# Kernel optimization log

Hardware: AMD Instinct MI355X
Metric: run time of the kernel (lower is better)

Reference implementation:

```python
import jax, jax.numpy as jnp
import numpy as np

MODEL_DIM = 1024
NUM_HEADS = 16
HEAD_DIM = MODEL_DIM // NUM_HEADS
B, N = 4, 2048


def setup_inputs() -> dict:
    key = jax.random.key(0)
    ks = jax.random.split(key, 6)
    s = 1.0 / np.sqrt(MODEL_DIM)
    x = jax.random.normal(ks[0], (B, N, MODEL_DIM), dtype=jnp.float32)
    Wq = jax.random.uniform(ks[1], (MODEL_DIM, MODEL_DIM), jnp.float32, -s, s)
    Wk = jax.random.uniform(ks[2], (MODEL_DIM, MODEL_DIM), jnp.float32, -s, s)
    Wv = jax.random.uniform(ks[3], (MODEL_DIM, MODEL_DIM), jnp.float32, -s, s)
    Wo = jax.random.uniform(ks[4], (MODEL_DIM, MODEL_DIM), jnp.float32, -s, s)
    bo = jax.random.uniform(ks[5], (MODEL_DIM,), jnp.float32, -s, s)
    return {"x": x, "Wq": Wq, "Wk": Wk, "Wv": Wv, "Wo": Wo, "bo": bo}


def reference(x, Wq, Wk, Wv, Wo, bo):
    # QKV projections (no bias), split heads: b n (h d) -> b h n d
    def split(t):
        b, n, _ = t.shape
        return t.reshape(b, n, NUM_HEADS, HEAD_DIM).transpose(0, 2, 1, 3)

    q = split(x @ Wq.T)
    k = split(x @ Wk.T)
    v = split(x @ Wv.T)

    scale = HEAD_DIM ** (-0.5)
    scores = jnp.einsum('bhnd,bhmd->bhnm', q, k) * scale  # [B,H,N,N]
    # causal mask (is_causal=True)
    causal = jnp.tril(jnp.ones((N, N), dtype=bool))
    scores = jnp.where(causal, scores, -jnp.inf)
    attn = jax.nn.softmax(scores, axis=-1)
    out = jnp.einsum('bhnm,bhmd->bhnd', attn, v)  # [B,H,N,D]
    out = out.transpose(0, 2, 1, 3).reshape(B, N, MODEL_DIM)
    return out @ Wo.T + bo
```

## Files before the change

### kernel.cpp

```cpp
#include <hip/hip_runtime.h>
#include <hip/hip_bf16.h>

typedef unsigned short u16;
typedef __attribute__((ext_vector_type(8))) __bf16 bf16x8;
typedef __attribute__((ext_vector_type(4))) float f32x4;
typedef __attribute__((ext_vector_type(2))) unsigned int u32x2;

#define MODEL_DIM 1024
#define NUM_HEADS 16
#define HEAD_DIM  64
#define BATCH     4
#define SEQ       2048
#define ROWS      (BATCH*SEQ)

static __device__ __forceinline__ u16 f2bf(float f) {
    union { __hip_bfloat16 h; u16 u; } cv;
    cv.h = __float2bfloat16(f);
    return cv.u;
}

static __device__ __forceinline__ void gload16(const u16* g, unsigned lds_byte) {
    __builtin_amdgcn_global_load_lds(
        (const __attribute__((address_space(1))) unsigned int*)g,
        (__attribute__((address_space(3))) unsigned int*)(uintptr_t)lds_byte,
        16, 0, 0);
}

__global__ void castk_all(const float* __restrict__ x,
                          const float* __restrict__ w0, const float* __restrict__ w1,
                          const float* __restrict__ w2, const float* __restrict__ w3,
                          u16* __restrict__ out) {
    const int total = ROWS * MODEL_DIM + 4 * MODEL_DIM * MODEL_DIM;
    int i = (blockIdx.x * blockDim.x + threadIdx.x) * 4;
    int stride = gridDim.x * blockDim.x * 4;
    for (; i < total; i += stride) {
        const float* src;
        int off;
        if (i < ROWS * MODEL_DIM) { src = x; off = i; }
        else {
            int j = i - ROWS * MODEL_DIM;
            int w = j >> 20;
            off = j & 1048575;
            src = (w == 0) ? w0 : (w == 1) ? w1 : (w == 2) ? w2 : w3;
        }
        float4 v = *reinterpret_cast<const float4*>(src + off);
        ushort4 o;
        o.x = f2bf(v.x); o.y = f2bf(v.y); o.z = f2bf(v.z); o.w = f2bf(v.w);
        *reinterpret_cast<ushort4*>(out + i) = o;
    }
}

#define BM 128
#define BN 128
#define BK 64
#define LDST 72

__global__ __launch_bounds__(256) void gemm_qkv(
    const u16* __restrict__ A,
    const u16* __restrict__ Wq, const u16* __restrict__ Wk, const u16* __restrict__ Wv,
    u16* __restrict__ qO, u16* __restrict__ kO, u16* __restrict__ vO)
{
    __shared__ u16 As[BM * LDST];
    __shared__ u16 Bs[BN * LDST];
    const int t    = threadIdx.x;
    const int wid  = t >> 6;
    const int lane = t & 63;
    const int lo   = lane & 15, hi = lane >> 4;
    const int bm   = blockIdx.x * BM;
    const int mat  = blockIdx.y >> 3;
    const int bn   = (blockIdx.y & 7) * BN;
    const u16* W   = (mat == 0) ? Wq : (mat == 1) ? Wk : Wv;
    u16* outB      = (mat == 0) ? qO : (mat == 1) ? kO : vO;
    const float qscale = (mat == 0) ? 0.18033688f : 1.0f;
    const int wr   = wid >> 1, wc = wid & 1;
    const int K = MODEL_DIM;

    f32x4 acc[4][4];
#pragma unroll
    for (int m = 0; m < 4; m++)
#pragma unroll
        for (int n = 0; n < 4; n++) acc[m][n] = (f32x4){0.f, 0.f, 0.f, 0.f};

    for (int k0 = 0; k0 < K; k0 += BK) {
        __syncthreads();
#pragma unroll
        for (int i = 0; i < 4; i++) {
            int a   = t + 256 * i;
            int row = a >> 3, ch = (a & 7) * 8;
            uint4 va = *reinterpret_cast<const uint4*>(A + (size_t)(bm + row) * K + k0 + ch);
            *reinterpret_cast<uint4*>(As + row * LDST + ch) = va;
            uint4 vb = *reinterpret_cast<const uint4*>(W + (size_t)(bn + row) * K + k0 + ch);
            *reinterpret_cast<uint4*>(Bs + row * LDST + ch) = vb;
        }
        __syncthreads();
#pragma unroll
        for (int h = 0; h < 2; h++) {
            bf16x8 af[4], bfr[4];
#pragma unroll
            for (int m = 0; m < 4; m++)
                af[m] = *reinterpret_cast<const bf16x8*>(As + (wr * 64 + m * 16 + lo) * LDST + h * 32 + hi * 8);
#pragma unroll
            for (int n = 0; n < 4; n++)
                bfr[n] = *reinterpret_cast<const bf16x8*>(Bs + (wc * 64 + n * 16 + lo) * LDST + h * 32 + hi * 8);
#pragma unroll
            for (int m = 0; m < 4; m++)
#pragma unroll
                for (int n = 0; n < 4; n++)
                    acc[m][n] = __builtin_amdgcn_mfma_f32_16x16x32_bf16(af[m], bfr[n], acc[m][n], 0, 0, 0);
        }
    }

#pragma unroll
    for (int m = 0; m < 4; m++)
#pragma unroll
        for (int n = 0; n < 4; n++)
#pragma unroll
            for (int r = 0; r < 4; r++) {
                int row = bm + wr * 64 + m * 16 + hi * 4 + r;
                int col = bn + wc * 64 + n * 16 + lo;
                int b = row >> 11, np = row & 2047;
                int hh = col >> 6, dd = col & 63;
                outB[(((size_t)(b * NUM_HEADS + hh) * SEQ + np) << 6) + dd] = f2bf(acc[m][n][r] * qscale);
            }
}

__global__ __launch_bounds__(256) void gemm_out(
    const u16* __restrict__ A,
    const u16* __restrict__ W,
    float* __restrict__ outF,
    const float* __restrict__ bias)
{
    __shared__ u16 As[BM * LDST];
    __shared__ u16 Bs[BN * LDST];
    const int t    = threadIdx.x;
    const int wid  = t >> 6;
    const int lane = t & 63;
    const int lo   = lane & 15, hi = lane >> 4;
    const int bm   = blockIdx.x * BM;
    const int bn   = blockIdx.y * BN;
    const int wr   = wid >> 1, wc = wid & 1;
    const int K = MODEL_DIM, N = MODEL_DIM;

    f32x4 acc[4][4];
#pragma unroll
    for (int m = 0; m < 4; m++)
#pragma unroll
        for (int n = 0; n < 4; n++) acc[m][n] = (f32x4){0.f, 0.f, 0.f, 0.f};

    for (int k0 = 0; k0 < K; k0 += BK) {
        __syncthreads();
#pragma unroll
        for (int i = 0; i < 4; i++) {
            int a   = t + 256 * i;
            int row = a >> 3, ch = (a & 7) * 8;
            uint4 va = *reinterpret_cast<const uint4*>(A + (size_t)(bm + row) * K + k0 + ch);
            *reinterpret_cast<uint4*>(As + row * LDST + ch) = va;
            uint4 vb = *reinterpret_cast<const uint4*>(W + (size_t)(bn + row) * K + k0 + ch);
            *reinterpret_cast<uint4*>(Bs + row * LDST + ch) = vb;
        }
        __syncthreads();
#pragma unroll
        for (int h = 0; h < 2; h++) {
            bf16x8 af[4], bfr[4];
#pragma unroll
            for (int m = 0; m < 4; m++)
                af[m] = *reinterpret_cast<const bf16x8*>(As + (wr * 64 + m * 16 + lo) * LDST + h * 32 + hi * 8);
#pragma unroll
            for (int n = 0; n < 4; n++)
                bfr[n] = *reinterpret_cast<const bf16x8*>(Bs + (wc * 64 + n * 16 + lo) * LDST + h * 32 + hi * 8);
#pragma unroll
            for (int m = 0; m < 4; m++)
#pragma unroll
                for (int n = 0; n < 4; n++)
                    acc[m][n] = __builtin_amdgcn_mfma_f32_16x16x32_bf16(af[m], bfr[n], acc[m][n], 0, 0, 0);
        }
    }

#pragma unroll
    for (int m = 0; m < 4; m++)
#pragma unroll
        for (int n = 0; n < 4; n++)
#pragma unroll
            for (int r = 0; r < 4; r++) {
                int row = bm + wr * 64 + m * 16 + hi * 4 + r;
                int col = bn + wc * 64 + n * 16 + lo;
                outF[(size_t)row * N + col] = acc[m][n][r] + bias[col];
            }
}


static __device__ __forceinline__ u32x2 tr16(unsigned int addr) {
    u32x2 r;
    asm volatile("ds_read_b64_tr_b16 %0, %1" : "=v"(r) : "v"(addr));
    return r;
}

__global__ __launch_bounds__(256, 8) void attn(
    const u16* __restrict__ Q,
    const u16* __restrict__ Kg,
    const u16* __restrict__ Vg,
    u16* __restrict__ O)
{
    __shared__ u16 lds[8192];
    const int t    = threadIdx.x;
    const int wid  = t >> 6, lane = t & 63;
    const int lo   = lane & 15, hi = lane >> 4;

    const int g    = blockIdx.x;
    const int slot = g >> 3;
    const int bh   = ((slot & 7) << 3) + (g & 7);
    const int a    = slot >> 3;
    const int u    = a >> 2, a0 = a & 3;
    const int qt   = 4 * u + ((u & 1) ? 3 - a0 : a0);

    const size_t base = (size_t)bh * SEQ * 64;
    const int qbase = qt * 64 + wid * 16;
    const unsigned ldsb = (unsigned)(uintptr_t)lds;

    int srcK[2], srcV[2];
    unsigned dstK[2], dstV[2];
#pragma unroll
    for (int ti = 0; ti < 2; ti++) {
        int o   = t * 8 + ti * 2048;
        int row = o >> 6;
        int colb = ((o & 63) * 2) ^ ((row & 7) << 4);
        srcK[ti] = row * 64 + (colb >> 1);
        dstK[ti] = ldsb + o * 2;
        int st = o >> 9;
        int kv = (st >> 2) * 32 + ((o >> 4) & 31);
        int d  = (st & 3) * 16 + (o & 15);
        srcV[ti] = kv * 64 + d;
        dstV[ti] = ldsb + 8192 + o * 2;
    }

    bf16x8 qf[2];
#pragma unroll
    for (int h = 0; h < 2; h++)
        qf[h] = *reinterpret_cast<const bf16x8*>(Q + base + (size_t)(qbase + lo) * 64 + h * 32 + hi * 8);
    asm volatile("" : "+v"(qf[0]), "+v"(qf[1]));

    float m_run = -3.0e38f, l_part = 0.f;
    f32x4 acc[4];
#pragma unroll
    for (int dt = 0; dt < 4; dt++) acc[dt] = (f32x4){0.f, 0.f, 0.f, 0.f};

    for (int j = 0; j <= qt; j++) {
        __builtin_amdgcn_s_barrier();
        {
            const u16* Kt = Kg + base + (size_t)j * 4096;
            const u16* Vt = Vg + base + (size_t)j * 4096;
#pragma unroll
            for (int ti = 0; ti < 2; ti++) {
                gload16(Kt + srcK[ti], dstK[ti]);
                gload16(Vt + srcV[ti], dstV[ti]);
            }
        }
        asm volatile("s_waitcnt vmcnt(0)" ::: "memory");
        __builtin_amdgcn_s_barrier();
        __builtin_amdgcn_sched_barrier(0);

        f32x4 s[4];
#pragma unroll
        for (int kh = 0; kh < 2; kh++) {
            bf16x8 kfa[2][2];
#pragma unroll
            for (int k2 = 0; k2 < 2; k2++)
#pragma unroll
                for (int h = 0; h < 2; h++)
                    kfa[k2][h] = *reinterpret_cast<const bf16x8*>(
                        (const char*)lds + ((kh * 2 + k2) * 16 + lo) * 128 + ((h * 64 + hi * 16) ^ ((lo & 7) << 4)));
            __builtin_amdgcn_s_setprio(1);
#pragma unroll
            for (int k2 = 0; k2 < 2; k2++) {
                f32x4 a2 = (f32x4){0.f, 0.f, 0.f, 0.f};
#pragma unroll
                for (int h = 0; h < 2; h++)
                    a2 = __builtin_amdgcn_mfma_f32_16x16x32_bf16(kfa[k2][h], qf[h], a2, 0, 0, 0);
                s[kh * 2 + k2] = a2;
            }
            __builtin_amdgcn_s_setprio(0);
        }
        if (j == qt) {
            const int ql = wid * 16 + lo;
#pragma unroll
            for (int kt = 0; kt < 4; kt++)
#pragma unroll
                for (int r = 0; r < 4; r++)
                    if (kt * 16 + hi * 4 + r > ql) s[kt][r] = -1.0e30f;
        }
        float vm = s[0][0];
#pragma unroll
        for (int kt = 0; kt < 4; kt++)
#pragma unroll
            for (int r = 0; r < 4; r++) vm = fmaxf(vm, s[kt][r]);
        vm = fmaxf(vm, __shfl_xor(vm, 16));
        vm = fmaxf(vm, __shfl_xor(vm, 32));
        if (!__all(vm <= m_run + 8.0f)) {
            float nm = fmaxf(m_run, vm);
            float sc = exp2f(m_run - nm);
            m_run = nm;
            l_part *= sc;
#pragma unroll
            for (int dt = 0; dt < 4; dt++)
#pragma unroll
                for (int r = 0; r < 4; r++) acc[dt][r] *= sc;
        }
        float ps = 0.f;
#pragma unroll
        for (int kt = 0; kt < 4; kt++)
#pragma unroll
            for (int r = 0; r < 4; r++) {
                float p = exp2f(s[kt][r] - m_run);
                s[kt][r] = p;
                ps += p;
            }
        l_part += ps;
        bf16x8 pa[2];
        {
            union { u16 uu[8]; bf16x8 v; } pk0, pk1;
#pragma unroll
            for (int e = 0; e < 4; e++) {
                pk0.uu[e]     = f2bf(s[0][e]);
                pk0.uu[4 + e] = f2bf(s[1][e]);
                pk1.uu[e]     = f2bf(s[2][e]);
                pk1.uu[4 + e] = f2bf(s[3][e]);
            }
            pa[0] = pk0.v;
            pa[1] = pk1.v;
        }

        const unsigned vtb = ldsb + 8192u + (unsigned)((hi * 64 + lo * 4) * 2);
#pragma unroll
        for (int pr = 0; pr < 2; pr++) {
            u32x2 tv[2][2][2];
#pragma unroll
            for (int d2 = 0; d2 < 2; d2++)
#pragma unroll
                for (int h = 0; h < 2; h++)
#pragma unroll
                    for (int sel = 0; sel < 2; sel++)
                        tv[d2][h][sel] = tr16(vtb + (unsigned)(((h * 4 + pr * 2 + d2) * 512 + sel * 256) * 2));
            asm volatile("s_waitcnt lgkmcnt(0)" ::: "memory");
            __builtin_amdgcn_sched_barrier(0);
            __builtin_amdgcn_s_setprio(1);
#pragma unroll
            for (int d2 = 0; d2 < 2; d2++) {
#pragma unroll
                for (int h = 0; h < 2; h++) {
                    union { unsigned int w[4]; bf16x8 v; } bv;
                    bv.w[0] = tv[d2][h][0][0];
                    bv.w[1] = tv[d2][h][0][1];
                    bv.w[2] = tv[d2][h][1][0];
                    bv.w[3] = tv[d2][h][1][1];
                    acc[pr * 2 + d2] = __builtin_amdgcn_mfma_f32_16x16x32_bf16(bv.v, pa[h], acc[pr * 2 + d2], 0, 0, 0);
                }
            }
            __builtin_amdgcn_s_setprio(0);
        }
    }

    float l = l_part;
    l += __shfl_xor(l, 16);
    l += __shfl_xor(l, 32);
    const float inv = 1.0f / l;
    const int b = bh >> 4, hh = bh & 15;
    const size_t orow = ((size_t)(b * SEQ + qbase + lo)) * 1024 + hh * 64;
#pragma unroll
    for (int dt = 0; dt < 4; dt++) {
        union { u16 uu[4]; uint2 d2; } pk;
#pragma unroll
        for (int r = 0; r < 4; r++) pk.uu[r] = f2bf(acc[dt][r] * inv);
        *reinterpret_cast<uint2*>(O + orow + dt * 16 + hi * 4) = pk.d2;
    }
}

extern "C" void kernel_launch(void* const* d_in, const int* in_sizes, int n_in,
                              void* d_out, int out_size, void* d_ws, size_t ws_size,
                              hipStream_t stream) {
    const float* x  = (const float*)d_in[0];
    const float* Wq = (const float*)d_in[1];
    const float* Wk = (const float*)d_in[2];
    const float* Wv = (const float*)d_in[3];
    const float* Wo = (const float*)d_in[4];
    const float* bo = (const float*)d_in[5];
    float* out = (float*)d_out;

    char* ws = (char*)d_ws;
    u16* xb  = (u16*)ws;
    u16* wqb = (u16*)(ws + 16777216);
    u16* wkb = wqb + 1048576;
    u16* wvb = wkb + 1048576;
    u16* wob = wvb + 1048576;
    u16* q   = (u16*)(ws + 16777216 + 8388608);
    u16* k   = q + 8388608;
    u16* v   = k + 8388608;
    u16* ao  = v + 8388608;

    castk_all<<<3072, 256, 0, stream>>>(x, Wq, Wk, Wv, Wo, xb);

    gemm_qkv<<<dim3(ROWS / BM, 24), 256, 0, stream>>>(xb, wqb, wkb, wvb, q, k, v);

    attn<<<2048, 256, 0, stream>>>(q, k, v, ao);

    gemm_out<<<dim3(ROWS / BM, MODEL_DIM / BN), 256, 0, stream>>>(ao, wob, out, bo);
}
```

Before: 190.5 us.

## Prefetch next KV tile into registers in attention; swizzled direct-to-LDS GEMM staging

The attention loop now loads the next K/V tile from global memory into registers before computing on the current tile, then writes those registers to LDS after a barrier. This hides global-load latency behind the QK/softmax/PV math, where before each iteration waited on vmcnt(0). The QKV and output GEMMs now stage A/B tiles with global_load_lds into an unpadded, XOR-swizzled LDS layout instead of loading through registers into padded rows. This cuts register round trips and avoids bank conflicts, at the cost of more live registers in attention and two barriers per iteration.

```diff
diff --git a/kernel.cpp b/kernel.cpp
--- a/kernel.cpp
+++ b/kernel.cpp
@@ -53,15 +53,31 @@
 #define BM 128
 #define BN 128
 #define BK 64
-#define LDST 72
+
+static __device__ __forceinline__ void stage_tile(const u16* gbase, int K,
+                                                  unsigned lds_byte_base, int t) {
+#pragma unroll
+    for (int ti = 0; ti < 4; ti++) {
+        int o    = t * 8 + ti * 2048;
+        int row  = o >> 6;
+        int colb = ((o & 63) * 2) ^ ((row & 7) << 4);
+        gload16(gbase + (size_t)row * K + (colb >> 1), lds_byte_base + o * 2);
+    }
+}
+
+static __device__ __forceinline__ bf16x8 frag_read(const char* base, int row, int h,
+                                                   int lo, int hi) {
+    return *reinterpret_cast<const bf16x8*>(
+        base + row * 128 + ((h * 64 + hi * 16) ^ ((lo & 7) << 4)));
+}
 
 __global__ __launch_bounds__(256) void gemm_qkv(
     const u16* __restrict__ A,
     const u16* __restrict__ Wq, const u16* __restrict__ Wk, const u16* __restrict__ Wv,
     u16* __restrict__ qO, u16* __restrict__ kO, u16* __restrict__ vO)
 {
-    __shared__ u16 As[BM * LDST];
-    __shared__ u16 Bs[BN * LDST];
+    __shared__ u16 As[BM * BK];
+    __shared__ u16 Bs[BN * BK];
     const int t    = threadIdx.x;
     const int wid  = t >> 6;
     const int lane = t & 63;
@@ -74,6 +90,8 @@
     const float qscale = (mat == 0) ? 0.18033688f : 1.0f;
     const int wr   = wid >> 1, wc = wid & 1;
     const int K = MODEL_DIM;
+    const unsigned AsB = (unsigned)(uintptr_t)As;
+    const unsigned BsB = (unsigned)(uintptr_t)Bs;
 
     f32x4 acc[4][4];
 #pragma unroll
@@ -83,25 +101,18 @@
 
     for (int k0 = 0; k0 < K; k0 += BK) {
         __syncthreads();
-#pragma unroll
-        for (int i = 0; i < 4; i++) {
-            int a   = t + 256 * i;
-            int row = a >> 3, ch = (a & 7) * 8;
-            uint4 va = *reinterpret_cast<const uint4*>(A + (size_t)(bm + row) * K + k0 + ch);
-            *reinterpret_cast<uint4*>(As + row * LDST + ch) = va;
-            uint4 vb = *reinterpret_cast<const uint4*>(W + (size_t)(bn + row) * K + k0 + ch);
-            *reinterpret_cast<uint4*>(Bs + row * LDST + ch) = vb;
-        }
+        stage_tile(A + (size_t)bm * K + k0, K, AsB, t);
+        stage_tile(W + (size_t)bn * K + k0, K, BsB, t);
         __syncthreads();
 #pragma unroll
         for (int h = 0; h < 2; h++) {
             bf16x8 af[4], bfr[4];
 #pragma unroll
             for (int m = 0; m < 4; m++)
-                af[m] = *reinterpret_cast<const bf16x8*>(As + (wr * 64 + m * 16 + lo) * LDST + h * 32 + hi * 8);
+                af[m] = frag_read((const char*)As, wr * 64 + m * 16 + lo, h, lo, hi);
 #pragma unroll
             for (int n = 0; n < 4; n++)
-                bfr[n] = *reinterpret_cast<const bf16x8*>(Bs + (wc * 64 + n * 16 + lo) * LDST + h * 32 + hi * 8);
+                bfr[n] = frag_read((const char*)Bs, wc * 64 + n * 16 + lo, h, lo, hi);
 #pragma unroll
             for (int m = 0; m < 4; m++)
 #pragma unroll
@@ -130,8 +141,8 @@
     float* __restrict__ outF,
     const float* __restrict__ bias)
 {
-    __shared__ u16 As[BM * LDST];
-    __shared__ u16 Bs[BN * LDST];
+    __shared__ u16 As[BM * BK];
+    __shared__ u16 Bs[BN * BK];
     const int t    = threadIdx.x;
     const int wid  = t >> 6;
     const int lane = t & 63;
@@ -140,6 +151,8 @@
     const int bn   = blockIdx.y * BN;
     const int wr   = wid >> 1, wc = wid & 1;
     const int K = MODEL_DIM, N = MODEL_DIM;
+    const unsigned AsB = (unsigned)(uintptr_t)As;
+    const unsigned BsB = (unsigned)(uintptr_t)Bs;
 
     f32x4 acc[4][4];
 #pragma unroll
@@ -149,25 +162,18 @@
 
     for (int k0 = 0; k0 < K; k0 += BK) {
         __syncthreads();
-#pragma unroll
-        for (int i = 0; i < 4; i++) {
-            int a   = t + 256 * i;
-            int row = a >> 3, ch = (a & 7) * 8;
-            uint4 va = *reinterpret_cast<const uint4*>(A + (size_t)(bm + row) * K + k0 + ch);
-            *reinterpret_cast<uint4*>(As + row * LDST + ch) = va;
-            uint4 vb = *reinterpret_cast<const uint4*>(W + (size_t)(bn + row) * K + k0 + ch);
-            *reinterpret_cast<uint4*>(Bs + row * LDST + ch) = vb;
-        }
+        stage_tile(A + (size_t)bm * K + k0, K, AsB, t);
+        stage_tile(W + (size_t)bn * K + k0, K, BsB, t);
         __syncthreads();
 #pragma unroll
         for (int h = 0; h < 2; h++) {
             bf16x8 af[4], bfr[4];
 #pragma unroll
             for (int m = 0; m < 4; m++)
-                af[m] = *reinterpret_cast<const bf16x8*>(As + (wr * 64 + m * 16 + lo) * LDST + h * 32 + hi * 8);
+                af[m] = frag_read((const char*)As, wr * 64 + m * 16 + lo, h, lo, hi);
 #pragma unroll
             for (int n = 0; n < 4; n++)
-                bfr[n] = *reinterpret_cast<const bf16x8*>(Bs + (wc * 64 + n * 16 + lo) * LDST + h * 32 + hi * 8);
+                bfr[n] = frag_read((const char*)Bs, wc * 64 + n * 16 + lo, h, lo, hi);
 #pragma unroll
             for (int m = 0; m < 4; m++)
 #pragma unroll
@@ -217,20 +223,20 @@
     const int qbase = qt * 64 + wid * 16;
     const unsigned ldsb = (unsigned)(uintptr_t)lds;
 
-    int srcK[2], srcV[2];
-    unsigned dstK[2], dstV[2];
+    int sK[2], sV[2];
+    unsigned dKb[2], dVb[2];
 #pragma unroll
     for (int ti = 0; ti < 2; ti++) {
         int o   = t * 8 + ti * 2048;
         int row = o >> 6;
         int colb = ((o & 63) * 2) ^ ((row & 7) << 4);
-        srcK[ti] = row * 64 + (colb >> 1);
-        dstK[ti] = ldsb + o * 2;
+        sK[ti] = row * 64 + (colb >> 1);
+        dKb[ti] = o * 2;
         int st = o >> 9;
         int kv = (st >> 2) * 32 + ((o >> 4) & 31);
         int d  = (st & 3) * 16 + (o & 15);
-        srcV[ti] = kv * 64 + d;
-        dstV[ti] = ldsb + 8192 + o * 2;
+        sV[ti] = kv * 64 + d;
+        dVb[ti] = 8192 + o * 2;
     }
 
     bf16x8 qf[2];
@@ -244,20 +250,31 @@
 #pragma unroll
     for (int dt = 0; dt < 4; dt++) acc[dt] = (f32x4){0.f, 0.f, 0.f, 0.f};
 
+    {
+        const u16* Kt = Kg + base;
+        const u16* Vt = Vg + base;
+        uint4 k0r = *reinterpret_cast<const uint4*>(Kt + sK[0]);
+        uint4 k1r = *reinterpret_cast<const uint4*>(Kt + sK[1]);
+        uint4 v0r = *reinterpret_cast<const uint4*>(Vt + sV[0]);
+        uint4 v1r = *reinterpret_cast<const uint4*>(Vt + sV[1]);
+        *reinterpret_cast<uint4*>((char*)lds + dKb[0]) = k0r;
+        *reinterpret_cast<uint4*>((char*)lds + dKb[1]) = k1r;
+        *reinterpret_cast<uint4*>((char*)lds + dVb[0]) = v0r;
+        *reinterpret_cast<uint4*>((char*)lds + dVb[1]) = v1r;
+    }
+
     for (int j = 0; j <= qt; j++) {
-        __builtin_amdgcn_s_barrier();
-        {
-            const u16* Kt = Kg + base + (size_t)j * 4096;
-            const u16* Vt = Vg + base + (size_t)j * 4096;
-#pragma unroll
-            for (int ti = 0; ti < 2; ti++) {
-                gload16(Kt + srcK[ti], dstK[ti]);
-                gload16(Vt + srcV[ti], dstV[ti]);
-            }
-        }
-        asm volatile("s_waitcnt vmcnt(0)" ::: "memory");
-        __builtin_amdgcn_s_barrier();
-        __builtin_amdgcn_sched_barrier(0);
+        uint4 pk0, pk1, pv0, pv1;
+        const bool pf = (j < qt);
+        if (pf) {
+            const u16* Kt = Kg + base + (size_t)(j + 1) * 4096;
+            const u16* Vt = Vg + base + (size_t)(j + 1) * 4096;
+            pk0 = *reinterpret_cast<const uint4*>(Kt + sK[0]);
+            pk1 = *reinterpret_cast<const uint4*>(Kt + sK[1]);
+            pv0 = *reinterpret_cast<const uint4*>(Vt + sV[0]);
+            pv1 = *reinterpret_cast<const uint4*>(Vt + sV[1]);
+        }
+        __syncthreads();
 
         f32x4 s[4];
 #pragma unroll
@@ -317,16 +334,16 @@
         l_part += ps;
         bf16x8 pa[2];
         {
-            union { u16 uu[8]; bf16x8 v; } pk0, pk1;
+            union { u16 uu[8]; bf16x8 v; } q0, q1;
 #pragma unroll
             for (int e = 0; e < 4; e++) {
-                pk0.uu[e]     = f2bf(s[0][e]);
-                pk0.uu[4 + e] = f2bf(s[1][e]);
-                pk1.uu[e]     = f2bf(s[2][e]);
-                pk1.uu[4 + e] = f2bf(s[3][e]);
-            }
-            pa[0] = pk0.v;
-            pa[1] = pk1.v;
+                q0.uu[e]     = f2bf(s[0][e]);
+                q0.uu[4 + e] = f2bf(s[1][e]);
+                q1.uu[e]     = f2bf(s[2][e]);
+                q1.uu[4 + e] = f2bf(s[3][e]);
+            }
+            pa[0] = q0.v;
+            pa[1] = q1.v;
         }
 
         const unsigned vtb = ldsb + 8192u + (unsigned)((hi * 64 + lo * 4) * 2);
@@ -356,6 +373,14 @@
                 }
             }
             __builtin_amdgcn_s_setprio(0);
+        }
+
+        __syncthreads();
+        if (pf) {
+            *reinterpret_cast<uint4*>((char*)lds + dKb[0]) = pk0;
+            *reinterpret_cast<uint4*>((char*)lds + dKb[1]) = pk1;
+            *reinterpret_cast<uint4*>((char*)lds + dVb[0]) = pv0;
+            *reinterpret_cast<uint4*>((char*)lds + dVb[1]) = pv1;
         }
     }
 
```

Result: slower. 445.3 us (+133.8%).

## Double-buffer GEMMs with async LDS loads and prefetch K/V tiles in attention

Applied to the files above, without the earlier changes.

Replaces the two register-staged GEMM kernels with one templated 256x128-tile, 512-thread GEMM. It loads tiles straight into XOR-swizzled LDS with global_load_lds and double-buffers them, so the next K-slice is fetched while MFMAs run on the current one. The attention kernel also double-buffers its K/V tiles, prefetching tile j+1 before computing on tile j. This doubles LDS use, so attention occupancy drops (launch bound lowered to 5) and the GEMM adds extra barriers per sub-step.

```diff
diff --git a/kernel.cpp b/kernel.cpp
--- a/kernel.cpp
+++ b/kernel.cpp
@@ -50,30 +50,64 @@
     }
 }
 
-#define BM 128
-#define BN 128
-#define BK 64
-#define LDST 72
-
-__global__ __launch_bounds__(256) void gemm_qkv(
+
+static __device__ __forceinline__ bf16x8 frag_read(const char* base, int row, int h,
+                                                   int lo, int hi) {
+    return *reinterpret_cast<const bf16x8*>(
+        base + row * 128 + ((h * 64 + hi * 16) ^ ((lo & 7) << 4)));
+}
+
+template<int EPI>
+__global__ __launch_bounds__(512, 2) void gemm_pipe(
     const u16* __restrict__ A,
     const u16* __restrict__ Wq, const u16* __restrict__ Wk, const u16* __restrict__ Wv,
-    u16* __restrict__ qO, u16* __restrict__ kO, u16* __restrict__ vO)
+    u16* __restrict__ qO, u16* __restrict__ kO, u16* __restrict__ vO,
+    float* __restrict__ outF, const float* __restrict__ bias)
 {
-    __shared__ u16 As[BM * LDST];
-    __shared__ u16 Bs[BN * LDST];
+    __shared__ u16 As[2 * 16384];
+    __shared__ u16 Bs[2 * 8192];
     const int t    = threadIdx.x;
     const int wid  = t >> 6;
     const int lane = t & 63;
     const int lo   = lane & 15, hi = lane >> 4;
-    const int bm   = blockIdx.x * BM;
-    const int mat  = blockIdx.y >> 3;
-    const int bn   = (blockIdx.y & 7) * BN;
-    const u16* W   = (mat == 0) ? Wq : (mat == 1) ? Wk : Wv;
-    u16* outB      = (mat == 0) ? qO : (mat == 1) ? kO : vO;
-    const float qscale = (mat == 0) ? 0.18033688f : 1.0f;
-    const int wr   = wid >> 1, wc = wid & 1;
+    const int bm   = blockIdx.x * 256;
+    int mat, bn;
+    const u16* W;
+    u16* outB = nullptr;
+    float qscale = 1.0f;
+    if (EPI == 0) {
+        mat = blockIdx.y >> 3;
+        bn  = (blockIdx.y & 7) * 128;
+        W   = (mat == 0) ? Wq : (mat == 1) ? Wk : Wv;
+        outB = (mat == 0) ? qO : (mat == 1) ? kO : vO;
+        qscale = (mat == 0) ? 0.18033688f : 1.0f;
+    } else {
+        bn = blockIdx.y * 128;
+        W  = Wq;
+    }
+    const int wr = wid >> 1, wc = wid & 1;
     const int K = MODEL_DIM;
+    const unsigned AsB = (unsigned)(uintptr_t)As;
+    const unsigned BsB = (unsigned)(uintptr_t)Bs;
+
+    const u16* aSrc[4]; unsigned aDst[4];
+    const u16* bSrc[2]; unsigned bDst[2];
+#pragma unroll
+    for (int ti = 0; ti < 4; ti++) {
+        int o = t * 8 + ti * 4096;
+        int row = o >> 6;
+        int colb = ((o & 63) * 2) ^ ((row & 7) << 4);
+        aSrc[ti] = A + (size_t)(bm + row) * K + (colb >> 1);
+        aDst[ti] = (unsigned)(o * 2);
+    }
+#pragma unroll
+    for (int ti = 0; ti < 2; ti++) {
+        int o = t * 8 + ti * 4096;
+        int row = o >> 6;
+        int colb = ((o & 63) * 2) ^ ((row & 7) << 4);
+        bSrc[ti] = W + (size_t)(bn + row) * K + (colb >> 1);
+        bDst[ti] = (unsigned)(o * 2);
+    }
 
     f32x4 acc[4][4];
 #pragma unroll
@@ -81,32 +115,51 @@
 #pragma unroll
         for (int n = 0; n < 4; n++) acc[m][n] = (f32x4){0.f, 0.f, 0.f, 0.f};
 
-    for (int k0 = 0; k0 < K; k0 += BK) {
-        __syncthreads();
-#pragma unroll
-        for (int i = 0; i < 4; i++) {
-            int a   = t + 256 * i;
-            int row = a >> 3, ch = (a & 7) * 8;
-            uint4 va = *reinterpret_cast<const uint4*>(A + (size_t)(bm + row) * K + k0 + ch);
-            *reinterpret_cast<uint4*>(As + row * LDST + ch) = va;
-            uint4 vb = *reinterpret_cast<const uint4*>(W + (size_t)(bn + row) * K + k0 + ch);
-            *reinterpret_cast<uint4*>(Bs + row * LDST + ch) = vb;
-        }
-        __syncthreads();
-#pragma unroll
-        for (int h = 0; h < 2; h++) {
-            bf16x8 af[4], bfr[4];
-#pragma unroll
-            for (int m = 0; m < 4; m++)
-                af[m] = *reinterpret_cast<const bf16x8*>(As + (wr * 64 + m * 16 + lo) * LDST + h * 32 + hi * 8);
+#pragma unroll
+    for (int ti = 0; ti < 4; ti++) gload16(aSrc[ti], AsB + aDst[ti]);
+#pragma unroll
+    for (int ti = 0; ti < 2; ti++) gload16(bSrc[ti], BsB + bDst[ti]);
+
+    for (int kt = 0; kt < 16; kt++) {
+        const int p = kt & 1;
+        if (kt < 15) {
+            const int ko = (kt + 1) * 64;
+            const unsigned pa = (unsigned)((p ^ 1) * 32768);
+            const unsigned pb = (unsigned)((p ^ 1) * 16384);
+#pragma unroll
+            for (int ti = 0; ti < 4; ti++) gload16(aSrc[ti] + ko, AsB + pa + aDst[ti]);
+#pragma unroll
+            for (int ti = 0; ti < 2; ti++) gload16(bSrc[ti] + ko, BsB + pb + bDst[ti]);
+            asm volatile("s_waitcnt vmcnt(6)" ::: "memory");
+        } else {
+            asm volatile("s_waitcnt vmcnt(0)" ::: "memory");
+        }
+        __builtin_amdgcn_s_barrier();
+        __builtin_amdgcn_sched_barrier(0);
+
+        const char* Ab = (const char*)As + p * 32768;
+        const char* Bb = (const char*)Bs + p * 16384;
+#pragma unroll
+        for (int kk = 0; kk < 2; kk++) {
+            bf16x8 bfr[4];
 #pragma unroll
             for (int n = 0; n < 4; n++)
-                bfr[n] = *reinterpret_cast<const bf16x8*>(Bs + (wc * 64 + n * 16 + lo) * LDST + h * 32 + hi * 8);
-#pragma unroll
-            for (int m = 0; m < 4; m++)
-#pragma unroll
-                for (int n = 0; n < 4; n++)
-                    acc[m][n] = __builtin_amdgcn_mfma_f32_16x16x32_bf16(af[m], bfr[n], acc[m][n], 0, 0, 0);
+                bfr[n] = frag_read(Bb, wc * 64 + n * 16 + lo, kk, lo, hi);
+#pragma unroll
+            for (int mh = 0; mh < 2; mh++) {
+                bf16x8 af[2];
+#pragma unroll
+                for (int m2 = 0; m2 < 2; m2++)
+                    af[m2] = frag_read(Ab, wr * 64 + (mh * 2 + m2) * 16 + lo, kk, lo, hi);
+                __builtin_amdgcn_s_setprio(1);
+#pragma unroll
+                for (int m2 = 0; m2 < 2; m2++)
+#pragma unroll
+                    for (int n = 0; n < 4; n++)
+                        acc[mh * 2 + m2][n] = __builtin_amdgcn_mfma_f32_16x16x32_bf16(af[m2], bfr[n], acc[mh * 2 + m2][n], 0, 0, 0);
+                __builtin_amdgcn_s_setprio(0);
+                __builtin_amdgcn_s_barrier();
+            }
         }
     }
 
@@ -118,73 +171,13 @@
             for (int r = 0; r < 4; r++) {
                 int row = bm + wr * 64 + m * 16 + hi * 4 + r;
                 int col = bn + wc * 64 + n * 16 + lo;
-                int b = row >> 11, np = row & 2047;
-                int hh = col >> 6, dd = col & 63;
-                outB[(((size_t)(b * NUM_HEADS + hh) * SEQ + np) << 6) + dd] = f2bf(acc[m][n][r] * qscale);
-            }
-}
-
-__global__ __launch_bounds__(256) void gemm_out(
-    const u16* __restrict__ A,
-    const u16* __restrict__ W,
-    float* __restrict__ outF,
-    const float* __restrict__ bias)
-{
-    __shared__ u16 As[BM * LDST];
-    __shared__ u16 Bs[BN * LDST];
-    const int t    = threadIdx.x;
-    const int wid  = t >> 6;
-    const int lane = t & 63;
-    const int lo   = lane & 15, hi = lane >> 4;
-    const int bm   = blockIdx.x * BM;
-    const int bn   = blockIdx.y * BN;
-    const int wr   = wid >> 1, wc = wid & 1;
-    const int K = MODEL_DIM, N = MODEL_DIM;
-
-    f32x4 acc[4][4];
-#pragma unroll
-    for (int m = 0; m < 4; m++)
-#pragma unroll
-        for (int n = 0; n < 4; n++) acc[m][n] = (f32x4){0.f, 0.f, 0.f, 0.f};
-
-    for (int k0 = 0; k0 < K; k0 += BK) {
-        __syncthreads();
-#pragma unroll
-        for (int i = 0; i < 4; i++) {
-            int a   = t + 256 * i;
-            int row = a >> 3, ch = (a & 7) * 8;
-            uint4 va = *reinterpret_cast<const uint4*>(A + (size_t)(bm + row) * K + k0 + ch);
-            *reinterpret_cast<uint4*>(As + row * LDST + ch) = va;
-            uint4 vb = *reinterpret_cast<const uint4*>(W + (size_t)(bn + row) * K + k0 + ch);
-            *reinterpret_cast<uint4*>(Bs + row * LDST + ch) = vb;
-        }
-        __syncthreads();
-#pragma unroll
-        for (int h = 0; h < 2; h++) {
-            bf16x8 af[4], bfr[4];
-#pragma unroll
-            for (int m = 0; m < 4; m++)
-                af[m] = *reinterpret_cast<const bf16x8*>(As + (wr * 64 + m * 16 + lo) * LDST + h * 32 + hi * 8);
-#pragma unroll
-            for (int n = 0; n < 4; n++)
-                bfr[n] = *reinterpret_cast<const bf16x8*>(Bs + (wc * 64 + n * 16 + lo) * LDST + h * 32 + hi * 8);
-#pragma unroll
-            for (int m = 0; m < 4; m++)
-#pragma unroll
-                for (int n = 0; n < 4; n++)
-                    acc[m][n] = __builtin_amdgcn_mfma_f32_16x16x32_bf16(af[m], bfr[n], acc[m][n], 0, 0, 0);
-        }
-    }
-
-#pragma unroll
-    for (int m = 0; m < 4; m++)
-#pragma unroll
-        for (int n = 0; n < 4; n++)
-#pragma unroll
-            for (int r = 0; r < 4; r++) {
-                int row = bm + wr * 64 + m * 16 + hi * 4 + r;
-                int col = bn + wc * 64 + n * 16 + lo;
-                outF[(size_t)row * N + col] = acc[m][n][r] + bias[col];
+                if (EPI == 0) {
+                    int b = row >> 11, np = row & 2047;
+                    int hh = col >> 6, dd = col & 63;
+                    outB[(((size_t)(b * NUM_HEADS + hh) * SEQ + np) << 6) + dd] = f2bf(acc[m][n][r] * qscale);
+                } else {
+                    outF[(size_t)row * MODEL_DIM + col] = acc[m][n][r] + bias[col];
+                }
             }
 }
 
@@ -195,13 +188,13 @@
     return r;
 }
 
-__global__ __launch_bounds__(256, 8) void attn(
+__global__ __launch_bounds__(256, 5) void attn(
     const u16* __restrict__ Q,
     const u16* __restrict__ Kg,
     const u16* __restrict__ Vg,
     u16* __restrict__ O)
 {
-    __shared__ u16 lds[8192];
+    __shared__ u16 lds[16384];
     const int t    = threadIdx.x;
     const int wid  = t >> 6, lane = t & 63;
     const int lo   = lane & 15, hi = lane >> 4;
@@ -230,7 +223,7 @@
         int kv = (st >> 2) * 32 + ((o >> 4) & 31);
         int d  = (st & 3) * 16 + (o & 15);
         srcV[ti] = kv * 64 + d;
-        dstV[ti] = ldsb + 8192 + o * 2;
+        dstV[ti] = ldsb + 8192u + o * 2;
     }
 
     bf16x8 qf[2];
@@ -244,21 +237,35 @@
 #pragma unroll
     for (int dt = 0; dt < 4; dt++) acc[dt] = (f32x4){0.f, 0.f, 0.f, 0.f};
 
+    {
+        const u16* Kt = Kg + base;
+        const u16* Vt = Vg + base;
+#pragma unroll
+        for (int ti = 0; ti < 2; ti++) {
+            gload16(Kt + srcK[ti], dstK[ti]);
+            gload16(Vt + srcV[ti], dstV[ti]);
+        }
+    }
+
     for (int j = 0; j <= qt; j++) {
-        __builtin_amdgcn_s_barrier();
-        {
-            const u16* Kt = Kg + base + (size_t)j * 4096;
-            const u16* Vt = Vg + base + (size_t)j * 4096;
+        const int p = j & 1;
+        if (j < qt) {
+            const u16* Kt = Kg + base + (size_t)(j + 1) * 4096;
+            const u16* Vt = Vg + base + (size_t)(j + 1) * 4096;
+            const unsigned bs = (unsigned)((p ^ 1) * 16384);
 #pragma unroll
             for (int ti = 0; ti < 2; ti++) {
-                gload16(Kt + srcK[ti], dstK[ti]);
-                gload16(Vt + srcV[ti], dstV[ti]);
-            }
-        }
-        asm volatile("s_waitcnt vmcnt(0)" ::: "memory");
+                gload16(Kt + srcK[ti], dstK[ti] + bs);
+                gload16(Vt + srcV[ti], dstV[ti] + bs);
+            }
+            asm volatile("s_waitcnt vmcnt(4)" ::: "memory");
+        } else {
+            asm volatile("s_waitcnt vmcnt(0)" ::: "memory");
+        }
         __builtin_amdgcn_s_barrier();
         __builtin_amdgcn_sched_barrier(0);
 
+        const char* Kcur = (const char*)lds + p * 16384;
         f32x4 s[4];
 #pragma unroll
         for (int kh = 0; kh < 2; kh++) {
@@ -268,7 +275,7 @@
 #pragma unroll
                 for (int h = 0; h < 2; h++)
                     kfa[k2][h] = *reinterpret_cast<const bf16x8*>(
-                        (const char*)lds + ((kh * 2 + k2) * 16 + lo) * 128 + ((h * 64 + hi * 16) ^ ((lo & 7) << 4)));
+                        Kcur + ((kh * 2 + k2) * 16 + lo) * 128 + ((h * 64 + hi * 16) ^ ((lo & 7) << 4)));
             __builtin_amdgcn_s_setprio(1);
 #pragma unroll
             for (int k2 = 0; k2 < 2; k2++) {
@@ -310,26 +317,26 @@
         for (int kt = 0; kt < 4; kt++)
 #pragma unroll
             for (int r = 0; r < 4; r++) {
-                float p = exp2f(s[kt][r] - m_run);
-                s[kt][r] = p;
-                ps += p;
+                float pv = exp2f(s[kt][r] - m_run);
+                s[kt][r] = pv;
+                ps += pv;
             }
         l_part += ps;
         bf16x8 pa[2];
         {
-            union { u16 uu[8]; bf16x8 v; } pk0, pk1;
+            union { u16 uu[8]; bf16x8 v; } q0, q1;
 #pragma unroll
             for (int e = 0; e < 4; e++) {
-                pk0.uu[e]     = f2bf(s[0][e]);
-                pk0.uu[4 + e] = f2bf(s[1][e]);
-                pk1.uu[e]     = f2bf(s[2][e]);
-                pk1.uu[4 + e] = f2bf(s[3][e]);
-            }
-            pa[0] = pk0.v;
-            pa[1] = pk1.v;
-        }
-
-        const unsigned vtb = ldsb + 8192u + (unsigned)((hi * 64 + lo * 4) * 2);
+                q0.uu[e]     = f2bf(s[0][e]);
+                q0.uu[4 + e] = f2bf(s[1][e]);
+                q1.uu[e]     = f2bf(s[2][e]);
+                q1.uu[4 + e] = f2bf(s[3][e]);
+            }
+            pa[0] = q0.v;
+            pa[1] = q1.v;
+        }
+
+        const unsigned vtb = ldsb + (unsigned)(p * 16384) + 8192u + (unsigned)((hi * 64 + lo * 4) * 2);
 #pragma unroll
         for (int pr = 0; pr < 2; pr++) {
             u32x2 tv[2][2][2];
@@ -357,6 +364,7 @@
             }
             __builtin_amdgcn_s_setprio(0);
         }
+        __builtin_amdgcn_s_barrier();
     }
 
     float l = l_part;
@@ -398,9 +406,11 @@
 
     castk_all<<<3072, 256, 0, stream>>>(x, Wq, Wk, Wv, Wo, xb);
 
-    gemm_qkv<<<dim3(ROWS / BM, 24), 256, 0, stream>>>(xb, wqb, wkb, wvb, q, k, v);
+    gemm_pipe<0><<<dim3(ROWS / 256, 24), 512, 0, stream>>>(
+        xb, wqb, wkb, wvb, q, k, v, nullptr, nullptr);
 
     attn<<<2048, 256, 0, stream>>>(q, k, v, ao);
 
-    gemm_out<<<dim3(ROWS / BM, MODEL_DIM / BN), 256, 0, stream>>>(ao, wob, out, bo);
-}
+    gemm_pipe<1><<<dim3(ROWS / 256, MODEL_DIM / 128), 512, 0, stream>>>(
+        ao, wob, nullptr, nullptr, nullptr, nullptr, nullptr, out, bo);
+}
```

Result: faster. 175.0 us (-8.1%).
